# Performance work log

Measured on AMD Instinct MI355X. Metric: run time of the kernel, lower is better.

## Reference

```python
import jax, jax.numpy as jnp
import numpy as np

N_NODES = 50000
N_EDGES = 800000
HEADS = 4
IN_CH = 128
HID_CH = 32   # per-head, conv1
OUT_CH = 32   # per-head, conv2
N_GRAPHS = 64
NEG_SLOPE = 0.2
BN_EPS = 1e-5


def gat_conv(x, src, dst, n_nodes, W, att_src, att_dst, bias):
    """PyG-style GATConv (concat heads). x:[N,Fin], W:[Fin,H*C], att_*:[H,C], bias:[H*C]."""
    H, C = att_src.shape
    h = (x @ W).reshape(n_nodes, H, C)                      # [N,H,C]
    a_src = jnp.einsum('nhc,hc->nh', h, att_src)            # [N,H]
    a_dst = jnp.einsum('nhc,hc->nh', h, att_dst)            # [N,H]
    e = jax.nn.leaky_relu(a_src[src] + a_dst[dst], NEG_SLOPE)  # [E,H]
    # segment softmax over incoming edges of each destination node
    e_max = jax.ops.segment_max(e, dst, num_segments=n_nodes)  # [N,H]
    alpha = jnp.exp(e - e_max[dst])                         # [E,H]
    denom = jax.ops.segment_sum(alpha, dst, num_segments=n_nodes)  # [N,H]
    alpha = alpha / denom[dst]
    msg = alpha[:, :, None] * h[src]                        # [E,H,C]
    out = jax.ops.segment_sum(msg, dst, num_segments=n_nodes)  # [N,H,C]
    return out.reshape(n_nodes, H * C) + bias


def setup_inputs() -> dict:
    key = jax.random.key(0)
    ks = jax.random.split(key, 12)
    d1 = HID_CH * HEADS  # 128
    d2 = OUT_CH * HEADS  # 128
    s_in = 1.0 / np.sqrt(IN_CH)
    s_h = 1.0 / np.sqrt(d1)
    return {
        'x': jax.random.normal(ks[0], (N_NODES, IN_CH), jnp.float32),
        'edge_index': jax.random.randint(ks[1], (2, N_EDGES), 0, N_NODES, jnp.int32),
        'batch': jnp.sort(jax.random.randint(ks[2], (N_NODES,), 0, N_GRAPHS, jnp.int32)),
        'W1': jax.random.normal(ks[3], (IN_CH, d1), jnp.float32) * s_in,
        'att_src1': jax.random.normal(ks[4], (HEADS, HID_CH), jnp.float32) * s_h,
        'att_dst1': jax.random.normal(ks[5], (HEADS, HID_CH), jnp.float32) * s_h,
        'bias1': jnp.zeros((d1,), jnp.float32),
        'gamma1': jnp.ones((d1,), jnp.float32),
        'beta1': jnp.zeros((d1,), jnp.float32),
        'W2': jax.random.normal(ks[6], (d1, d2), jnp.float32) * s_h,
        'att_src2': jax.random.normal(ks[7], (HEADS, OUT_CH), jnp.float32) * s_h,
        'att_dst2': jax.random.normal(ks[8], (HEADS, OUT_CH), jnp.float32) * s_h,
        'bias2': jnp.zeros((d2,), jnp.float32),
    }


def reference(x, edge_index, batch, W1, att_src1, att_dst1, bias1,
              gamma1, beta1, W2, att_src2, att_dst2, bias2):
    n = x.shape[0]
    loops = jnp.arange(n, dtype=edge_index.dtype)
    src = jnp.concatenate([edge_index[0], loops])  # add self-loops (PyG default)
    dst = jnp.concatenate([edge_index[1], loops])

    h = gat_conv(x, src, dst, n, W1, att_src1, att_dst1, bias1)
    # BatchNorm1d (batch statistics, biased variance), then ELU; dropout is inference no-op
    mu = h.mean(axis=0)
    var = h.var(axis=0)
    h = (h - mu) * jax.lax.rsqrt(var + BN_EPS) * gamma1 + beta1
    h = jax.nn.elu(h)

    h2 = gat_conv(h, src, dst, n, W2, att_src2, att_dst2, bias2)  # [N, OUT_CH*HEADS]

    # global mean pool over graphs
    ones = jnp.ones((n,), h2.dtype)
    counts = jax.ops.segment_sum(ones, batch, num_segments=N_GRAPHS)
    pooled = jax.ops.segment_sum(h2, batch, num_segments=N_GRAPHS)
    graph_rep = pooled / jnp.maximum(counts, 1.0)[:, None]
    return (h2, graph_rep)
```

## Files before the change

kernel.cpp:

```cpp
#include <hip/hip_runtime.h>

#define NN 50000
#define NE 800000
#define ET 850000
#define NG 64
#define D  128
#define NB 196
#define CAP 5120
#define CHUNK 8192

typedef unsigned short u16;
typedef unsigned int   u32;
typedef short bf16x8 __attribute__((ext_vector_type(8)));
typedef float f32x4  __attribute__((ext_vector_type(4)));

__device__ __forceinline__ u16 f2b(float f){
  u32 u = __float_as_uint(f);
  u32 r = (u + 0x7fffu + ((u >> 16) & 1u)) >> 16;
  return (u16)r;
}
__device__ __forceinline__ u32 pack2(float a, float b){
  return (u32)f2b(a) | ((u32)f2b(b) << 16);
}
__device__ __forceinline__ float lo16f(u32 u){ return __uint_as_float(u << 16); }
__device__ __forceinline__ float hi16f(u32 u){ return __uint_as_float(u & 0xffff0000u); }

__global__ void k_init(int* gCur, float* bsum, float* bsq, float* pooled,
                       const float* __restrict__ W1, const float* __restrict__ W2,
                       u16* __restrict__ WTb1, u16* __restrict__ WTb2){
  int i = blockIdx.x*256 + threadIdx.x;
  if (i < 256) gCur[i] = 0;
  if (i < 128){ bsum[i] = 0.f; bsq[i] = 0.f; }
  if (i < NG*D) pooled[i] = 0.f;
  if (i < D*D){
    int c = i >> 7, k = i & 127;
    WTb1[i] = f2b(W1[(size_t)k*D + c]);
    WTb2[i] = f2b(W2[(size_t)k*D + c]);
  }
}

__global__ __launch_bounds__(256) void k_bucket(const int* __restrict__ srcE, const int* __restrict__ dstE,
                                                int* __restrict__ gCur, int* __restrict__ temp){
  __shared__ int hist[256], hbase[256], hpos[256], gbase[256];
  __shared__ int sorted[CHUNK];
  int tid = threadIdx.x;
  int e0 = blockIdx.x * CHUNK;
  int e1 = e0 + CHUNK; if (e1 > NE) e1 = NE;
  int cnt = e1 - e0;
  hist[tid] = 0;
  __syncthreads();
  for (int i = e0 + tid; i < e1; i += 256)
    atomicAdd(&hist[(u32)dstE[i] >> 8], 1);
  __syncthreads();
  int v = hist[tid];
  hbase[tid] = v;
  __syncthreads();
  for (int off = 1; off < 256; off <<= 1){
    int t = (tid >= off) ? hbase[tid-off] : 0;
    __syncthreads();
    hbase[tid] += t;
    __syncthreads();
  }
  int excl = hbase[tid] - v;
  __syncthreads();
  hbase[tid] = excl;
  hpos[tid]  = excl;
  __syncthreads();
  for (int i = e0 + tid; i < e1; i += 256){
    int d = dstE[i], sr = srcE[i];
    int idx = atomicAdd(&hpos[(u32)d >> 8], 1);
    sorted[idx] = (d << 16) | sr;
  }
  __syncthreads();
  if (tid < NB && hist[tid] > 0)
    gbase[tid] = atomicAdd(&gCur[tid], hist[tid]);
  __syncthreads();
  for (int i = tid; i < cnt; i += 256){
    int vv = sorted[i];
    int b = (u32)vv >> 24;
    int pos = gbase[b] + (i - hbase[b]);
    if (pos < CAP) temp[b*CAP + pos] = vv;
  }
}

__global__ void k_bstart(const int* __restrict__ gCur, int* __restrict__ bstart, int* __restrict__ offs){
  __shared__ int s[256];
  int tid = threadIdx.x;
  int nodes = (tid < NB) ? ((tid == NB-1) ? (NN - (NB-1)*256) : 256) : 0;
  int v = (tid < NB) ? gCur[tid] + nodes : 0;
  s[tid] = v;
  __syncthreads();
  for (int off = 1; off < 256; off <<= 1){
    int t = (tid >= off) ? s[tid-off] : 0;
    __syncthreads();
    s[tid] += t;
    __syncthreads();
  }
  if (tid < NB) bstart[tid] = s[tid] - v;
  if (tid == 0) offs[NN] = ET;
}

__global__ __launch_bounds__(256) void k_place(const int* __restrict__ temp, const int* __restrict__ gCur,
                                               const int* __restrict__ bstart, int* __restrict__ offs,
                                               int* __restrict__ srcs){
  __shared__ int cnt256[256], pfx[256], pos[256];
  int b = blockIdx.x, tid = threadIdx.x;
  int n0 = b << 8;
  int nNodes = NN - n0; if (nNodes > 256) nNodes = 256;
  int count = gCur[b];
  const int* tb = temp + b*CAP;
  cnt256[tid] = 0;
  __syncthreads();
  for (int i = tid; i < count; i += 256)
    atomicAdd(&cnt256[((u32)tb[i] >> 16) & 255], 1);
  __syncthreads();
  int own = cnt256[tid] + (tid < nNodes ? 1 : 0);
  pfx[tid] = own;
  __syncthreads();
  for (int off = 1; off < 256; off <<= 1){
    int t = (tid >= off) ? pfx[tid-off] : 0;
    __syncthreads();
    pfx[tid] += t;
    __syncthreads();
  }
  int excl = pfx[tid] - own;
  __syncthreads();
  pos[tid] = excl + 1;
  __syncthreads();
  int base = bstart[b];
  if (tid < nNodes){
    offs[n0 + tid] = base + excl;
    srcs[base + excl] = n0 + tid;
  }
  for (int i = tid; i < count; i += 256){
    int vv = tb[i];
    int d = ((u32)vv >> 16) & 255;
    int k = atomicAdd(&pos[d], 1);
    srcs[base + k] = vv & 0xFFFF;
  }
}

template<int FUSE_BN>
__global__ __launch_bounds__(512) void k_gemm(const float* __restrict__ X, const u16* __restrict__ WTb,
                                              u16* __restrict__ Ybf,
                                              const float* __restrict__ att_s, const float* __restrict__ att_d,
                                              float* __restrict__ asrc, float* __restrict__ adst,
                                              const float* __restrict__ bsc, const float* __restrict__ bsh,
                                              int nrows){
  __shared__ u16 Xs[128*136];
  __shared__ u16 WT[128*136];
  int tid = threadIdx.x;
  int row0 = blockIdx.x * 128;
  #pragma unroll
  for (int t = 0; t < 8; t++){
    int i = tid + t*512;
    int r = i >> 5, k4 = i & 31;
    int gr = row0 + r;
    float4 v = (gr < nrows) ? ((const float4*)(X + (size_t)gr*D))[k4]
                            : make_float4(0.f,0.f,0.f,0.f);
    if (FUSE_BN){
      float4 sc = ((const float4*)bsc)[k4];
      float4 sh = ((const float4*)bsh)[k4];
      v.x = fmaf(v.x, sc.x, sh.x); v.y = fmaf(v.y, sc.y, sh.y);
      v.z = fmaf(v.z, sc.z, sh.z); v.w = fmaf(v.w, sc.w, sh.w);
      v.x = v.x > 0.f ? v.x : expm1f(v.x);
      v.y = v.y > 0.f ? v.y : expm1f(v.y);
      v.z = v.z > 0.f ? v.z : expm1f(v.z);
      v.w = v.w > 0.f ? v.w : expm1f(v.w);
    }
    *(uint2*)&Xs[r*136 + k4*4] = make_uint2(pack2(v.x, v.y), pack2(v.z, v.w));
  }
  #pragma unroll
  for (int t = 0; t < 4; t++){
    int i = tid + t*512;
    int c = i >> 4, k16 = i & 15;
    uint4 vv = ((const uint4*)WTb)[i];
    *(uint4*)&WT[c*136 + k16*8] = vv;
  }
  __syncthreads();
  int w = tid >> 6, l = tid & 63;
  int l15 = l & 15, lq = l >> 4;
  int cw = w*16;
  bf16x8 bfr[4];
  #pragma unroll
  for (int ks = 0; ks < 4; ks++)
    bfr[ks] = *(const bf16x8*)&WT[(cw + l15)*136 + ks*32 + lq*8];
  f32x4 acc[8];
  #pragma unroll
  for (int m = 0; m < 8; m++) acc[m] = (f32x4){0.f,0.f,0.f,0.f};
  #pragma unroll
  for (int m = 0; m < 8; m++){
    #pragma unroll
    for (int ks = 0; ks < 4; ks++){
      bf16x8 af = *(const bf16x8*)&Xs[(m*16 + l15)*136 + ks*32 + lq*8];
      acc[m] = __builtin_amdgcn_mfma_f32_16x16x32_bf16(af, bfr[ks], acc[m], 0, 0, 0);
    }
  }
  __syncthreads();
  float* sDotS = (float*)Xs;
  float* sDotD = sDotS + 1024;
  {
    float as_c = att_s[cw + l15];
    float ad_c = att_d[cw + l15];
    #pragma unroll
    for (int m = 0; m < 8; m++){
      #pragma unroll
      for (int i = 0; i < 4; i++){
        float ps = acc[m][i] * as_c;
        float pd = acc[m][i] * ad_c;
        #pragma unroll
        for (int msk = 1; msk <= 8; msk <<= 1){
          ps += __shfl_xor(ps, msk);
          pd += __shfl_xor(pd, msk);
        }
        if (l15 == 0){
          int r = m*16 + lq*4 + i;
          sDotS[w*128 + r] = ps;
          sDotD[w*128 + r] = pd;
        }
      }
    }
  }
  #pragma unroll
  for (int m = 0; m < 8; m++){
    #pragma unroll
    for (int i = 0; i < 4; i++){
      float v = acc[m][i];
      float nb = __shfl_xor(v, 1);
      if (!(l & 1)){
        int gr = row0 + m*16 + lq*4 + i;
        if (gr < nrows)
          *(u32*)&Ybf[(size_t)gr*D + cw + l15] = pack2(v, nb);
      }
    }
  }
  __syncthreads();
  {
    int r = tid >> 2, h = tid & 3;
    int gr = row0 + r;
    if (gr < nrows){
      asrc[gr*4 + h] = sDotS[(2*h)*128 + r] + sDotS[(2*h+1)*128 + r];
      adst[gr*4 + h] = sDotD[(2*h)*128 + r] + sDotD[(2*h+1)*128 + r];
    }
  }
}

__global__ __launch_bounds__(256) void k_edge(
                       const u16* __restrict__ hb, const float* __restrict__ asrc,
                       const float* __restrict__ adst, const int* __restrict__ offs,
                       const int* __restrict__ srcs, const float* __restrict__ bias,
                       float* __restrict__ out){
  __shared__ uint2 sPk[4][4][17];
  int w = threadIdx.x >> 6;
  int lane = threadIdx.x & 63;
  int n = blockIdx.x*4 + w;
  int off0 = offs[n];
  int deg  = offs[n+1] - off0;
  int hd = lane >> 4, j16 = lane & 15;
  float adh = adst[n*4 + hd];
  int half = lane >> 5, q = lane & 31;
  int hg = q >> 3;
  int qb = q*8;
  float denp = 0.f;
  float acc0=0.f, acc1=0.f, acc2=0.f, acc3=0.f;
  const char* hbase = (const char*)hb;
  const int* sp = srcs + off0;
  int sj = (j16 < deg) ? sp[j16] : 0;
  float av = asrc[sj*4 + hd];
  for (int base = 0; base < deg; base += 16){
    int lim = deg - base; if (lim > 16) lim = 16;
    int nbase = base + 16;
    bool hasn = (nbase < deg);
    int sjn = 0;
    if (hasn){
      int idx = nbase + j16;
      sjn = (idx < deg) ? sp[idx] : 0;
    }
    float al;
    if (j16 < lim){
      float e = av + adh;
      e = e > 0.f ? e : 0.2f*e;
      al = __expf(e);
    } else al = 0.f;
    denp += al;
    sPk[w][hd][j16] = make_uint2((u32)sj << 8, __float_as_uint(al));
    float avn = hasn ? asrc[sjn*4 + hd] : 0.f;
    if (lim == 16){
      uint2 p0 = sPk[w][hg][half],      p1 = sPk[w][hg][2+half];
      uint2 p2 = sPk[w][hg][4+half],    p3 = sPk[w][hg][6+half];
      uint2 p4 = sPk[w][hg][8+half],    p5 = sPk[w][hg][10+half];
      uint2 p6 = sPk[w][hg][12+half],   p7 = sPk[w][hg][14+half];
      uint2 v0 = *(const uint2*)(hbase + p0.x + qb);
      uint2 v1 = *(const uint2*)(hbase + p1.x + qb);
      uint2 v2 = *(const uint2*)(hbase + p2.x + qb);
      uint2 v3 = *(const uint2*)(hbase + p3.x + qb);
      uint2 v4 = *(const uint2*)(hbase + p4.x + qb);
      uint2 v5 = *(const uint2*)(hbase + p5.x + qb);
      uint2 v6 = *(const uint2*)(hbase + p6.x + qb);
      uint2 v7 = *(const uint2*)(hbase + p7.x + qb);
      float a0 = __uint_as_float(p0.y), a1 = __uint_as_float(p1.y);
      float a2 = __uint_as_float(p2.y), a3 = __uint_as_float(p3.y);
      float a4 = __uint_as_float(p4.y), a5 = __uint_as_float(p5.y);
      float a6 = __uint_as_float(p6.y), a7 = __uint_as_float(p7.y);
      acc0 = fmaf(a0, lo16f(v0.x), acc0); acc1 = fmaf(a0, hi16f(v0.x), acc1);
      acc2 = fmaf(a0, lo16f(v0.y), acc2); acc3 = fmaf(a0, hi16f(v0.y), acc3);
      acc0 = fmaf(a1, lo16f(v1.x), acc0); acc1 = fmaf(a1, hi16f(v1.x), acc1);
      acc2 = fmaf(a1, lo16f(v1.y), acc2); acc3 = fmaf(a1, hi16f(v1.y), acc3);
      acc0 = fmaf(a2, lo16f(v2.x), acc0); acc1 = fmaf(a2, hi16f(v2.x), acc1);
      acc2 = fmaf(a2, lo16f(v2.y), acc2); acc3 = fmaf(a2, hi16f(v2.y), acc3);
      acc0 = fmaf(a3, lo16f(v3.x), acc0); acc1 = fmaf(a3, hi16f(v3.x), acc1);
      acc2 = fmaf(a3, lo16f(v3.y), acc2); acc3 = fmaf(a3, hi16f(v3.y), acc3);
      acc0 = fmaf(a4, lo16f(v4.x), acc0); acc1 = fmaf(a4, hi16f(v4.x), acc1);
      acc2 = fmaf(a4, lo16f(v4.y), acc2); acc3 = fmaf(a4, hi16f(v4.y), acc3);
      acc0 = fmaf(a5, lo16f(v5.x), acc0); acc1 = fmaf(a5, hi16f(v5.x), acc1);
      acc2 = fmaf(a5, lo16f(v5.y), acc2); acc3 = fmaf(a5, hi16f(v5.y), acc3);
      acc0 = fmaf(a6, lo16f(v6.x), acc0); acc1 = fmaf(a6, hi16f(v6.x), acc1);
      acc2 = fmaf(a6, lo16f(v6.y), acc2); acc3 = fmaf(a6, hi16f(v6.y), acc3);
      acc0 = fmaf(a7, lo16f(v7.x), acc0); acc1 = fmaf(a7, hi16f(v7.x), acc1);
      acc2 = fmaf(a7, lo16f(v7.y), acc2); acc3 = fmaf(a7, hi16f(v7.y), acc3);
    } else {
      for (int j = 0; j < lim; j += 8){
        uint2 pA = sPk[w][hg][j+half],   pB = sPk[w][hg][j+2+half];
        uint2 pC = sPk[w][hg][j+4+half], pD = sPk[w][hg][j+6+half];
        uint2 vA = *(const uint2*)(hbase + pA.x + qb);
        uint2 vB = *(const uint2*)(hbase + pB.x + qb);
        uint2 vC = *(const uint2*)(hbase + pC.x + qb);
        uint2 vD = *(const uint2*)(hbase + pD.x + qb);
        float aA = __uint_as_float(pA.y), aB = __uint_as_float(pB.y);
        float aC = __uint_as_float(pC.y), aD = __uint_as_float(pD.y);
        acc0 = fmaf(aA, lo16f(vA.x), acc0); acc1 = fmaf(aA, hi16f(vA.x), acc1);
        acc2 = fmaf(aA, lo16f(vA.y), acc2); acc3 = fmaf(aA, hi16f(vA.y), acc3);
        acc0 = fmaf(aB, lo16f(vB.x), acc0); acc1 = fmaf(aB, hi16f(vB.x), acc1);
        acc2 = fmaf(aB, lo16f(vB.y), acc2); acc3 = fmaf(aB, hi16f(vB.y), acc3);
        acc0 = fmaf(aC, lo16f(vC.x), acc0); acc1 = fmaf(aC, hi16f(vC.x), acc1);
        acc2 = fmaf(aC, lo16f(vC.y), acc2); acc3 = fmaf(aC, hi16f(vC.y), acc3);
        acc0 = fmaf(aD, lo16f(vD.x), acc0); acc1 = fmaf(aD, hi16f(vD.x), acc1);
        acc2 = fmaf(aD, lo16f(vD.y), acc2); acc3 = fmaf(aD, hi16f(vD.y), acc3);
      }
    }
    sj = sjn; av = avn;
  }
  denp += __shfl_xor(denp, 1);
  denp += __shfl_xor(denp, 2);
  denp += __shfl_xor(denp, 4);
  denp += __shfl_xor(denp, 8);
  acc0 += __shfl_xor(acc0, 32);
  acc1 += __shfl_xor(acc1, 32);
  acc2 += __shfl_xor(acc2, 32);
  acc3 += __shfl_xor(acc3, 32);
  float inv = 1.f / __shfl(denp, hg*16);
  if (half == 0){
    int cb = q*4;
    float4 o;
    o.x = acc0*inv + bias[cb];
    o.y = acc1*inv + bias[cb+1];
    o.z = acc2*inv + bias[cb+2];
    o.w = acc3*inv + bias[cb+3];
    ((float4*)(out + (size_t)n*D))[q] = o;
  }
}

__global__ __launch_bounds__(256) void k_bnstat(const float* __restrict__ B,
                                                float* __restrict__ bsum, float* __restrict__ bsq){
  __shared__ float sS[256], sQ[256];
  int tid = threadIdx.x;
  int c = tid & 127;
  int rr = tid >> 7;
  int r0 = blockIdx.x * 64;
  int r1 = r0 + 64; if (r1 > NN) r1 = NN;
  float s = 0.f, qv = 0.f;
  for (int r = r0 + rr; r < r1; r += 2){
    float v = B[(size_t)r*D + c];
    s += v; qv += v*v;
  }
  sS[tid] = s; sQ[tid] = qv;
  __syncthreads();
  if (tid < 128){
    atomicAdd(&bsum[c], sS[tid] + sS[tid+128]);
    atomicAdd(&bsq[c],  sQ[tid] + sQ[tid+128]);
  }
}

__global__ void k_bnfin(const float* __restrict__ bsum, const float* __restrict__ bsq,
                        const float* __restrict__ gamma, const float* __restrict__ beta,
                        float* __restrict__ scale, float* __restrict__ shift){
  int c = threadIdx.x;
  float mu  = bsum[c] * (1.f/NN);
  float var = bsq[c] * (1.f/NN) - mu*mu;
  float sc  = gamma[c] * rsqrtf(var + 1e-5f);
  scale[c] = sc;
  shift[c] = beta[c] - mu*sc;
}

#define POOL_ROWS 50
__global__ void k_poolA(const float* __restrict__ h2, const int* __restrict__ batch,
                        float* __restrict__ pooled){
  int c = threadIdx.x & 127;
  int half = threadIdx.x >> 7;
  int r0 = blockIdx.x * POOL_ROWS;
  int r1 = r0 + POOL_ROWS; if (r1 > NN) r1 = NN;
  float s = 0.f; int g = -1;
  for (int r = r0 + half; r < r1; r += 2){
    int bg = batch[r];
    if (bg != g){
      if (g >= 0) atomicAdd(&pooled[g*D + c], s);
      g = bg; s = 0.f;
    }
    s += h2[(size_t)r*D + c];
  }
  if (g >= 0) atomicAdd(&pooled[g*D + c], s);
}

__global__ void k_poolB(const float* __restrict__ pooled, const int* __restrict__ batch,
                        float* __restrict__ out){
  int g = blockIdx.x;
  int c = threadIdx.x;
  int lo = 0, hi = NN;
  while (lo < hi){ int mid = (lo+hi) >> 1; if (batch[mid] < g) lo = mid+1; else hi = mid; }
  int a = lo, b = NN;
  while (a < b){ int mid = (a+b) >> 1; if (batch[mid] < g+1) a = mid+1; else b = mid; }
  int cntg = a - lo;
  out[g*D + c] = pooled[g*D + c] / (float)(cntg > 1 ? cntg : 1);
}

extern "C" void kernel_launch(void* const* d_in, const int* in_sizes, int n_in,
                              void* d_out, int out_size, void* d_ws, size_t ws_size,
                              hipStream_t stream){
  (void)in_sizes; (void)n_in; (void)out_size; (void)ws_size;
  const float* x   = (const float*)d_in[0];
  const int* ei    = (const int*)d_in[1];
  const int* batch = (const int*)d_in[2];
  const float* W1  = (const float*)d_in[3];
  const float* as1 = (const float*)d_in[4];
  const float* ad1 = (const float*)d_in[5];
  const float* b1  = (const float*)d_in[6];
  const float* g1  = (const float*)d_in[7];
  const float* be1 = (const float*)d_in[8];
  const float* W2  = (const float*)d_in[9];
  const float* as2 = (const float*)d_in[10];
  const float* ad2 = (const float*)d_in[11];
  const float* b2  = (const float*)d_in[12];
  float* outp = (float*)d_out;

  float* B    = (float*)d_ws;
  float* asr  = B + 6400000;
  float* ads  = asr + 200000;
  float* bsum = ads + 200000;
  float* bsq  = bsum + 128;
  float* bsc  = bsq + 128;
  float* bsh  = bsc + 128;
  float* pooled = bsh + 128;
  int* gCur   = (int*)(pooled + NG*D);
  int* bstart = gCur + 256;
  int* offs   = bstart + 256;
  int* srcs   = offs + (NN+1);
  int* temp   = srcs + ET;
  u16* hb     = (u16*)(temp + NB*CAP);
  u16* WTb1   = hb + 6400000;
  u16* WTb2   = WTb1 + D*D;

  const int* srcE = ei;
  const int* dstE = ei + NE;

  k_init<<<64, 256, 0, stream>>>(gCur, bsum, bsq, pooled, W1, W2, WTb1, WTb2);
  k_gemm<0><<<391, 512, 0, stream>>>(x, WTb1, hb, as1, ad1, asr, ads, nullptr, nullptr, NN);
  k_bucket<<<(NE + CHUNK - 1)/CHUNK, 256, 0, stream>>>(srcE, dstE, gCur, temp);
  k_bstart<<<1, 256, 0, stream>>>(gCur, bstart, offs);
  k_place<<<NB, 256, 0, stream>>>(temp, gCur, bstart, offs, srcs);
  k_edge<<<NN/4, 256, 0, stream>>>(hb, asr, ads, offs, srcs, b1, B);
  k_bnstat<<<782, 256, 0, stream>>>(B, bsum, bsq);
  k_bnfin<<<1, 128, 0, stream>>>(bsum, bsq, g1, be1, bsc, bsh);
  k_gemm<1><<<391, 512, 0, stream>>>(B, WTb2, hb, as2, ad2, asr, ads, bsc, bsh, NN);
  k_edge<<<NN/4, 256, 0, stream>>>(hb, asr, ads, offs, srcs, b2, outp);
  k_poolA<<<(NN + POOL_ROWS - 1)/POOL_ROWS, 256, 0, stream>>>(outp, batch, pooled);
  k_poolB<<<NG, 128, 0, stream>>>(pooled, batch, outp + 6400000);
}
```

Baseline: 232.4 us.

## Store layer-1 output in bf16 and fold small scan and BN-finalize kernels

The first GAT layer's output is now written as bf16 instead of fp32, and both the BatchNorm statistics kernel and the second GEMM read that half-size buffer. The block-start prefix scan moves into k_place, with every block redoing the 196-entry scan, and the BN finalize step moves into the prologue of the second GEMM. This cuts the memory traffic of the intermediate activations and removes two tiny kernel launches. The cost is that BN statistics are computed from bf16-rounded values, and each place block repeats a small scan.

```diff
diff --git a/kernel.cpp b/kernel.cpp
--- a/kernel.cpp
+++ b/kernel.cpp
@@ -83,28 +83,22 @@
   }
 }
 
-__global__ void k_bstart(const int* __restrict__ gCur, int* __restrict__ bstart, int* __restrict__ offs){
-  __shared__ int s[256];
-  int tid = threadIdx.x;
-  int nodes = (tid < NB) ? ((tid == NB-1) ? (NN - (NB-1)*256) : 256) : 0;
-  int v = (tid < NB) ? gCur[tid] + nodes : 0;
-  s[tid] = v;
+__global__ __launch_bounds__(256) void k_place(const int* __restrict__ temp, const int* __restrict__ gCur,
+                                               int* __restrict__ offs, int* __restrict__ srcs){
+  __shared__ int cnt256[256], pfx[256], pos[256], sb[256];
+  int b = blockIdx.x, tid = threadIdx.x;
+  int nodes_i = (tid < NB) ? ((tid == NB-1) ? (NN - (NB-1)*256) : 256) : 0;
+  int bv = (tid < NB) ? gCur[tid] + nodes_i : 0;
+  sb[tid] = bv;
   __syncthreads();
   for (int off = 1; off < 256; off <<= 1){
-    int t = (tid >= off) ? s[tid-off] : 0;
-    __syncthreads();
-    s[tid] += t;
-    __syncthreads();
-  }
-  if (tid < NB) bstart[tid] = s[tid] - v;
-  if (tid == 0) offs[NN] = ET;
-}
-
-__global__ __launch_bounds__(256) void k_place(const int* __restrict__ temp, const int* __restrict__ gCur,
-                                               const int* __restrict__ bstart, int* __restrict__ offs,
-                                               int* __restrict__ srcs){
-  __shared__ int cnt256[256], pfx[256], pos[256];
-  int b = blockIdx.x, tid = threadIdx.x;
+    int t = (tid >= off) ? sb[tid-off] : 0;
+    __syncthreads();
+    sb[tid] += t;
+    __syncthreads();
+  }
+  int base = (b == 0) ? 0 : sb[b-1];
+  if (b == 0 && tid == 0) offs[NN] = ET;
   int n0 = b << 8;
   int nNodes = NN - n0; if (nNodes > 256) nNodes = 256;
   int count = gCur[b];
@@ -127,7 +121,6 @@
   __syncthreads();
   pos[tid] = excl + 1;
   __syncthreads();
-  int base = bstart[b];
   if (tid < nNodes){
     offs[n0 + tid] = base + excl;
     srcs[base + excl] = n0 + tid;
@@ -141,34 +134,61 @@
 }
 
 template<int FUSE_BN>
-__global__ __launch_bounds__(512) void k_gemm(const float* __restrict__ X, const u16* __restrict__ WTb,
+__global__ __launch_bounds__(512) void k_gemm(const float* __restrict__ Xf, const u16* __restrict__ Xb,
+                                              const u16* __restrict__ WTb,
                                               u16* __restrict__ Ybf,
                                               const float* __restrict__ att_s, const float* __restrict__ att_d,
                                               float* __restrict__ asrc, float* __restrict__ adst,
-                                              const float* __restrict__ bsc, const float* __restrict__ bsh,
+                                              const float* __restrict__ bsum, const float* __restrict__ bsq,
+                                              const float* __restrict__ gamma, const float* __restrict__ beta,
                                               int nrows){
   __shared__ u16 Xs[128*136];
   __shared__ u16 WT[128*136];
+  __shared__ float sBsc[128], sBsh[128];
   int tid = threadIdx.x;
   int row0 = blockIdx.x * 128;
-  #pragma unroll
-  for (int t = 0; t < 8; t++){
-    int i = tid + t*512;
-    int r = i >> 5, k4 = i & 31;
-    int gr = row0 + r;
-    float4 v = (gr < nrows) ? ((const float4*)(X + (size_t)gr*D))[k4]
-                            : make_float4(0.f,0.f,0.f,0.f);
-    if (FUSE_BN){
-      float4 sc = ((const float4*)bsc)[k4];
-      float4 sh = ((const float4*)bsh)[k4];
-      v.x = fmaf(v.x, sc.x, sh.x); v.y = fmaf(v.y, sc.y, sh.y);
-      v.z = fmaf(v.z, sc.z, sh.z); v.w = fmaf(v.w, sc.w, sh.w);
-      v.x = v.x > 0.f ? v.x : expm1f(v.x);
-      v.y = v.y > 0.f ? v.y : expm1f(v.y);
-      v.z = v.z > 0.f ? v.z : expm1f(v.z);
-      v.w = v.w > 0.f ? v.w : expm1f(v.w);
-    }
-    *(uint2*)&Xs[r*136 + k4*4] = make_uint2(pack2(v.x, v.y), pack2(v.z, v.w));
+  if (FUSE_BN){
+    if (tid < 128){
+      float mu  = bsum[tid] * (1.f/NN);
+      float var = bsq[tid] * (1.f/NN) - mu*mu;
+      float sc  = gamma[tid] * rsqrtf(var + 1e-5f);
+      sBsc[tid] = sc;
+      sBsh[tid] = beta[tid] - mu*sc;
+    }
+    __syncthreads();
+  }
+  if (FUSE_BN){
+    #pragma unroll
+    for (int t = 0; t < 8; t++){
+      int i = tid + t*512;
+      int r = i >> 5, c4 = i & 31;
+      int gr = row0 + r;
+      uint2 o = make_uint2(0u, 0u);
+      if (gr < nrows){
+        uint2 u = ((const uint2*)Xb)[(size_t)gr*32 + c4];
+        float v0 = lo16f(u.x), v1 = hi16f(u.x), v2 = lo16f(u.y), v3 = hi16f(u.y);
+        float4 sc = ((const float4*)sBsc)[c4];
+        float4 sh = ((const float4*)sBsh)[c4];
+        v0 = fmaf(v0, sc.x, sh.x); v1 = fmaf(v1, sc.y, sh.y);
+        v2 = fmaf(v2, sc.z, sh.z); v3 = fmaf(v3, sc.w, sh.w);
+        v0 = v0 > 0.f ? v0 : expm1f(v0);
+        v1 = v1 > 0.f ? v1 : expm1f(v1);
+        v2 = v2 > 0.f ? v2 : expm1f(v2);
+        v3 = v3 > 0.f ? v3 : expm1f(v3);
+        o = make_uint2(pack2(v0, v1), pack2(v2, v3));
+      }
+      *(uint2*)&Xs[r*136 + c4*4] = o;
+    }
+  } else {
+    #pragma unroll
+    for (int t = 0; t < 8; t++){
+      int i = tid + t*512;
+      int r = i >> 5, k4 = i & 31;
+      int gr = row0 + r;
+      float4 v = (gr < nrows) ? ((const float4*)(Xf + (size_t)gr*D))[k4]
+                              : make_float4(0.f,0.f,0.f,0.f);
+      *(uint2*)&Xs[r*136 + k4*4] = make_uint2(pack2(v.x, v.y), pack2(v.z, v.w));
+    }
   }
   #pragma unroll
   for (int t = 0; t < 4; t++){
@@ -245,11 +265,12 @@
   }
 }
 
+template<int BF16OUT>
 __global__ __launch_bounds__(256) void k_edge(
                        const u16* __restrict__ hb, const float* __restrict__ asrc,
                        const float* __restrict__ adst, const int* __restrict__ offs,
                        const int* __restrict__ srcs, const float* __restrict__ bias,
-                       float* __restrict__ out){
+                       float* __restrict__ outf, u16* __restrict__ outb){
   __shared__ uint2 sPk[4][4][17];
   int w = threadIdx.x >> 6;
   int lane = threadIdx.x & 63;
@@ -351,45 +372,44 @@
   float inv = 1.f / __shfl(denp, hg*16);
   if (half == 0){
     int cb = q*4;
-    float4 o;
-    o.x = acc0*inv + bias[cb];
-    o.y = acc1*inv + bias[cb+1];
-    o.z = acc2*inv + bias[cb+2];
-    o.w = acc3*inv + bias[cb+3];
-    ((float4*)(out + (size_t)n*D))[q] = o;
-  }
-}
-
-__global__ __launch_bounds__(256) void k_bnstat(const float* __restrict__ B,
+    float o0 = acc0*inv + bias[cb];
+    float o1 = acc1*inv + bias[cb+1];
+    float o2 = acc2*inv + bias[cb+2];
+    float o3 = acc3*inv + bias[cb+3];
+    if (BF16OUT){
+      *(uint2*)(outb + (size_t)n*D + cb) = make_uint2(pack2(o0, o1), pack2(o2, o3));
+    } else {
+      ((float4*)(outf + (size_t)n*D))[q] = make_float4(o0, o1, o2, o3);
+    }
+  }
+}
+
+__global__ __launch_bounds__(256) void k_bnstat(const u16* __restrict__ Bb,
                                                 float* __restrict__ bsum, float* __restrict__ bsq){
-  __shared__ float sS[256], sQ[256];
+  __shared__ float sS0[256], sS1[256], sQ0[256], sQ1[256];
   int tid = threadIdx.x;
-  int c = tid & 127;
-  int rr = tid >> 7;
+  int c2 = tid & 63, rr = tid >> 6;
   int r0 = blockIdx.x * 64;
   int r1 = r0 + 64; if (r1 > NN) r1 = NN;
-  float s = 0.f, qv = 0.f;
-  for (int r = r0 + rr; r < r1; r += 2){
-    float v = B[(size_t)r*D + c];
-    s += v; qv += v*v;
-  }
-  sS[tid] = s; sQ[tid] = qv;
-  __syncthreads();
-  if (tid < 128){
-    atomicAdd(&bsum[c], sS[tid] + sS[tid+128]);
-    atomicAdd(&bsq[c],  sQ[tid] + sQ[tid+128]);
-  }
-}
-
-__global__ void k_bnfin(const float* __restrict__ bsum, const float* __restrict__ bsq,
-                        const float* __restrict__ gamma, const float* __restrict__ beta,
-                        float* __restrict__ scale, float* __restrict__ shift){
-  int c = threadIdx.x;
-  float mu  = bsum[c] * (1.f/NN);
-  float var = bsq[c] * (1.f/NN) - mu*mu;
-  float sc  = gamma[c] * rsqrtf(var + 1e-5f);
-  scale[c] = sc;
-  shift[c] = beta[c] - mu*sc;
+  const u32* Bp = (const u32*)Bb;
+  float s0 = 0.f, s1 = 0.f, q0 = 0.f, q1 = 0.f;
+  for (int r = r0 + rr; r < r1; r += 4){
+    u32 u = Bp[(size_t)r*64 + c2];
+    float v0 = lo16f(u), v1 = hi16f(u);
+    s0 += v0; s1 += v1; q0 += v0*v0; q1 += v1*v1;
+  }
+  sS0[tid] = s0; sS1[tid] = s1; sQ0[tid] = q0; sQ1[tid] = q1;
+  __syncthreads();
+  if (tid < 64){
+    s0 = sS0[tid] + sS0[tid+64] + sS0[tid+128] + sS0[tid+192];
+    s1 = sS1[tid] + sS1[tid+64] + sS1[tid+128] + sS1[tid+192];
+    q0 = sQ0[tid] + sQ0[tid+64] + sQ0[tid+128] + sQ0[tid+192];
+    q1 = sQ1[tid] + sQ1[tid+64] + sQ1[tid+128] + sQ1[tid+192];
+    atomicAdd(&bsum[2*tid],   s0);
+    atomicAdd(&bsum[2*tid+1], s1);
+    atomicAdd(&bsq[2*tid],    q0);
+    atomicAdd(&bsq[2*tid+1],  q1);
+  }
 }
 
 #define POOL_ROWS 50
@@ -442,36 +462,33 @@
   const float* b2  = (const float*)d_in[12];
   float* outp = (float*)d_out;
 
-  float* B    = (float*)d_ws;
-  float* asr  = B + 6400000;
+  float* asr  = (float*)d_ws;
   float* ads  = asr + 200000;
   float* bsum = ads + 200000;
   float* bsq  = bsum + 128;
-  float* bsc  = bsq + 128;
-  float* bsh  = bsc + 128;
-  float* pooled = bsh + 128;
+  float* pooled = bsq + 128;
   int* gCur   = (int*)(pooled + NG*D);
-  int* bstart = gCur + 256;
-  int* offs   = bstart + 256;
+  int* offs   = gCur + 256;
   int* srcs   = offs + (NN+1);
   int* temp   = srcs + ET;
   u16* hb     = (u16*)(temp + NB*CAP);
-  u16* WTb1   = hb + 6400000;
+  u16* Bb     = hb + 6400000;
+  u16* WTb1   = Bb + 6400000;
   u16* WTb2   = WTb1 + D*D;
 
   const int* srcE = ei;
   const int* dstE = ei + NE;
 
   k_init<<<64, 256, 0, stream>>>(gCur, bsum, bsq, pooled, W1, W2, WTb1, WTb2);
-  k_gemm<0><<<391, 512, 0, stream>>>(x, WTb1, hb, as1, ad1, asr, ads, nullptr, nullptr, NN);
+  k_gemm<0><<<391, 512, 0, stream>>>(x, nullptr, WTb1, hb, as1, ad1, asr, ads,
+                                     nullptr, nullptr, nullptr, nullptr, NN);
   k_bucket<<<(NE + CHUNK - 1)/CHUNK, 256, 0, stream>>>(srcE, dstE, gCur, temp);
-  k_bstart<<<1, 256, 0, stream>>>(gCur, bstart, offs);
-  k_place<<<NB, 256, 0, stream>>>(temp, gCur, bstart, offs, srcs);
-  k_edge<<<NN/4, 256, 0, stream>>>(hb, asr, ads, offs, srcs, b1, B);
-  k_bnstat<<<782, 256, 0, stream>>>(B, bsum, bsq);
-  k_bnfin<<<1, 128, 0, stream>>>(bsum, bsq, g1, be1, bsc, bsh);
-  k_gemm<1><<<391, 512, 0, stream>>>(B, WTb2, hb, as2, ad2, asr, ads, bsc, bsh, NN);
-  k_edge<<<NN/4, 256, 0, stream>>>(hb, asr, ads, offs, srcs, b2, outp);
+  k_place<<<NB, 256, 0, stream>>>(temp, gCur, offs, srcs);
+  k_edge<1><<<NN/4, 256, 0, stream>>>(hb, asr, ads, offs, srcs, b1, nullptr, Bb);
+  k_bnstat<<<782, 256, 0, stream>>>(Bb, bsum, bsq);
+  k_gemm<1><<<391, 512, 0, stream>>>(nullptr, Bb, WTb2, hb, as2, ad2, asr, ads,
+                                     bsum, bsq, g1, be1, NN);
+  k_edge<0><<<NN/4, 256, 0, stream>>>(hb, asr, ads, offs, srcs, b2, outp, nullptr);
   k_poolA<<<(NN + POOL_ROWS - 1)/POOL_ROWS, 256, 0, stream>>>(outp, batch, pooled);
   k_poolB<<<NG, 128, 0, stream>>>(pooled, batch, outp + 6400000);
 }
```

Measured after the change: 245.2 us. +5.5%, slower.
